# Kernel tuning notes

Hardware: AMD Instinct MI355X
Metric: run time of the kernel (lower is better)

## Reference

```python
import jax, jax.numpy as jnp
import numpy as np

B, S, D, H = 2, 2048, 1024, 16
DH = D // H
CBS, STRIDE = 32, 16      # compress block size / sliding stride
NSEL = 16                 # num_selected_blocks
WIN = 16                  # sliding_window_size (half-width)
SCALE = DH ** -0.5


def setup_inputs() -> dict:
    key = jax.random.key(0)
    ks = jax.random.split(key, 12)
    s = 0.02
    return {
        "x": jax.random.normal(ks[0], (B, S, D), jnp.float32),
        "qkv_w": jax.random.normal(ks[1], (D, 3 * D), jnp.float32) * s,
        "qkv_b": jnp.zeros((3 * D,), jnp.float32),
        "c1_w": jax.random.normal(ks[2], (CBS * D, D), jnp.float32) * s,
        "c1_b": jnp.zeros((D,), jnp.float32),
        "c2_w": jax.random.normal(ks[3], (D, D), jnp.float32) * s,
        "c2_b": jnp.zeros((D,), jnp.float32),
        "score_w": jax.random.normal(ks[4], (D, 1), jnp.float32) * s,
        "score_b": jnp.zeros((1,), jnp.float32),
        "out_w": jax.random.normal(ks[5], (D, D), jnp.float32) * s,
        "out_b": jnp.zeros((D,), jnp.float32),
    }


def reference(x, qkv_w, qkv_b, c1_w, c1_b, c2_w, c2_b, score_w, score_b, out_w, out_b):
    # q, k, v: [B, H, S, DH]
    qkv = (x @ qkv_w + qkv_b).reshape(B, S, 3, H, DH).transpose(2, 0, 3, 1, 4)
    q, k, v = qkv[0], qkv[1], qkv[2]

    # --- token compression: overlapping blocks -> MLP ---
    starts = jnp.arange(0, S - CBS + 1, STRIDE)                 # [nb]
    blk_idx = starts[:, None] + jnp.arange(CBS)[None, :]        # [nb, CBS]
    blocks = x[:, blk_idx, :].reshape(B, starts.shape[0], CBS * D)
    hidden = jax.nn.relu(blocks @ c1_w + c1_b)
    compressed = hidden @ c2_w + c2_b                           # [B, nb, D]

    # --- block selection via learned scores + top-k ---
    scores = (compressed @ score_w + score_b)[..., 0]           # [B, nb]
    _, top_idx = jax.lax.top_k(scores, NSEL)                    # [B, NSEL]
    selected = jnp.take_along_axis(compressed, top_idx[:, :, None], axis=1)  # [B, NSEL, D]

    sqkv = (selected @ qkv_w + qkv_b).reshape(B, NSEL, 3, H, DH).transpose(2, 0, 3, 1, 4)
    sel_k, sel_v = sqkv[1], sqkv[2]                             # [B, H, NSEL, DH]

    # --- sliding-window local attention (vectorized gather of banded K/V) ---
    offs = jnp.arange(-WIN, WIN + 1)                            # [2W+1]
    pos = jnp.arange(S)[:, None] + offs[None, :]                # [S, 2W+1]
    valid = (pos >= 0) & (pos < S)
    pos_c = jnp.clip(pos, 0, S - 1)
    kw = k[:, :, pos_c, :]                                      # [B, H, S, 2W+1, DH]
    vw = v[:, :, pos_c, :]
    sc = jnp.einsum('bhsd,bhswd->bhsw', q, kw) * SCALE
    sc = jnp.where(valid[None, None], sc, -jnp.inf)
    local = jnp.einsum('bhsw,bhswd->bhsd', jax.nn.softmax(sc, axis=-1), vw)

    # --- global attention over selected compressed blocks ---
    gsc = jnp.einsum('bhsd,bhkd->bhsk', q, sel_k) * SCALE       # [B, H, S, NSEL]
    glob = jnp.einsum('bhsk,bhkd->bhsd', jax.nn.softmax(gsc, axis=-1), sel_v)

    out = (local + glob).transpose(0, 2, 1, 3).reshape(B, S, D)
    return out @ out_w + out_b
```

## Files before the change

### kernel.cpp

```cpp
#include <hip/hip_runtime.h>
#include <math.h>

#define BB   2
#define SS   2048
#define DD   1024
#define HH   16
#define DH   64
#define CBS  32
#define STRIDEC 16
#define NBLK 127
#define NSEL 16
#define WIN  16
#define NW   33
#define SCALE 0.125f
#define MC   254

typedef _Float16 f16;
typedef __attribute__((ext_vector_type(8))) _Float16 f16x8;
typedef __attribute__((ext_vector_type(4))) _Float16 f16x4;
typedef __attribute__((ext_vector_type(2))) _Float16 h2;
typedef __attribute__((ext_vector_type(4))) float f32x4;

__global__ __launch_bounds__(256) void convert_f16(
    const float* __restrict__ src, f16* __restrict__ dst, int n)
{
    const int i = (blockIdx.x * 256 + threadIdx.x) * 4;
    if (i >= n) return;
    float4 v = *(const float4*)(src + i);
    f16x4 o;
    o[0] = (f16)v.x; o[1] = (f16)v.y; o[2] = (f16)v.z; o[3] = (f16)v.w;
    *(f16x4*)(dst + i) = o;
}

__global__ __launch_bounds__(256) void transpose_conv(
    const float* __restrict__ src, f16* __restrict__ dst, int K, int N)
{
    __shared__ float t[32][33];
    const int n0 = blockIdx.x * 32, k0 = blockIdx.y * 32;
    const int tx = threadIdx.x & 31, ty = threadIdx.x >> 5;
#pragma unroll
    for (int r = 0; r < 32; r += 8)
        t[ty + r][tx] = src[(size_t)(k0 + ty + r) * N + n0 + tx];
    __syncthreads();
#pragma unroll
    for (int r = 0; r < 32; r += 8)
        dst[(size_t)(n0 + ty + r) * K + k0 + tx] = (f16)t[tx][ty + r];
}

template<int OUT16>
__global__ __launch_bounds__(256) void gemm_f16(
    const f16* __restrict__ A, const f16* __restrict__ Bt,
    const float* __restrict__ bias, float* __restrict__ C,
    int M, int N, int K)
{
    constexpr int BK = 64;
    __shared__ f16 As[128 * BK];
    __shared__ f16 Bs[128 * BK];
    const int tid  = threadIdx.x;
    const int wid  = tid >> 6, lane = tid & 63;
    const int bm = blockIdx.y * 128, bn = blockIdx.x * 128;
    const int wm = (wid >> 1) * 64, wn = (wid & 1) * 64;

    const int lrow = lane >> 3;
    const int lk8  = (lane & 7) * 8;

    f32x4 acc[4][4];
#pragma unroll
    for (int i = 0; i < 4; ++i)
#pragma unroll
        for (int j = 0; j < 4; ++j) acc[i][j] = (f32x4){0.f, 0.f, 0.f, 0.f};

    for (int kt = 0; kt < K; kt += BK) {
#pragma unroll
        for (int c = 0; c < 4; ++c) {
            const int seg = c * 4 + wid;
            const int row = seg * 8 + lrow;
            const f16* ga = A + (size_t)(bm + row) * K + kt + lk8;
            __builtin_amdgcn_global_load_lds(
                (const __attribute__((address_space(1))) void*)(const void*)ga,
                (__attribute__((address_space(3))) void*)(void*)(As + seg * 512),
                16, 0, 0);
            const f16* gb = Bt + (size_t)(bn + row) * K + kt + lk8;
            __builtin_amdgcn_global_load_lds(
                (const __attribute__((address_space(1))) void*)(const void*)gb,
                (__attribute__((address_space(3))) void*)(void*)(Bs + seg * 512),
                16, 0, 0);
        }
        __syncthreads();

#pragma unroll
        for (int kk = 0; kk < 2; ++kk) {
            const int ko = kk * 32 + (lane >> 4) * 8;
            f16x8 a[4], b[4];
#pragma unroll
            for (int i = 0; i < 4; ++i)
                a[i] = *(const f16x8*)(As + (wm + i * 16 + (lane & 15)) * BK + ko);
#pragma unroll
            for (int j = 0; j < 4; ++j)
                b[j] = *(const f16x8*)(Bs + (wn + j * 16 + (lane & 15)) * BK + ko);
#pragma unroll
            for (int i = 0; i < 4; ++i)
#pragma unroll
                for (int j = 0; j < 4; ++j)
                    acc[i][j] = __builtin_amdgcn_mfma_f32_16x16x32_f16(
                        a[i], b[j], acc[i][j], 0, 0, 0);
        }
        __syncthreads();
    }

    const int rr0 = (lane >> 4) * 4;
    const int cc  = lane & 15;
#pragma unroll
    for (int i = 0; i < 4; ++i) {
        const int r = bm + wm + i * 16 + rr0;
#pragma unroll
        for (int j = 0; j < 4; ++j) {
            const int cn = bn + wn + j * 16 + cc;
            const float bv = bias[cn];
#pragma unroll
            for (int q = 0; q < 4; ++q) {
                if constexpr (OUT16)
                    ((f16*)C)[(size_t)(r + q) * N + cn] = (f16)(acc[i][j][q] + bv);
                else
                    C[(size_t)(r + q) * N + cn] = acc[i][j][q] + bv;
            }
        }
    }
}

#define C1_NZ 32
#define C1_KCHUNK 1024

__global__ __launch_bounds__(512) void gemm_c1(
    const f16* __restrict__ xh, const float* __restrict__ c1w,
    float* __restrict__ P)
{
    constexpr int BK = 64;
    constexpr int BSTR = 72;
    __shared__ f16 As[256 * BK];
    __shared__ f16 Bs[64 * BSTR];
    const int tid  = threadIdx.x;
    const int wid  = tid >> 6, lane = tid & 63;
    const int bn = blockIdx.x * 64;
    const int z  = blockIdx.z;
    const int wm = wid * 32;

    const int lrow = lane >> 3;
    const int lk8  = (lane & 7) * 8;

    f32x4 acc[2][4];
#pragma unroll
    for (int i = 0; i < 2; ++i)
#pragma unroll
        for (int j = 0; j < 4; ++j) acc[i][j] = (f32x4){0.f, 0.f, 0.f, 0.f};

    for (int t = 0; t < C1_KCHUNK / BK; ++t) {
        const int ktg = z * C1_KCHUNK + t * BK;
        const int kc  = (ktg + lk8) >> 10;
        const int kd  = (ktg + lk8) & 1023;
#pragma unroll
        for (int c = 0; c < 4; ++c) {
            const int seg = c * 8 + wid;
            int row = seg * 8 + lrow;
            if (row > MC - 1) row = MC - 1;
            const int b   = (row >= NBLK) ? 1 : 0;
            const int blk = row - b * NBLK;
            const f16* ga = xh + ((size_t)(b * SS + blk * STRIDEC + kc) << 10) + kd;
            __builtin_amdgcn_global_load_lds(
                (const __attribute__((address_space(1))) void*)(const void*)ga,
                (__attribute__((address_space(3))) void*)(void*)(As + seg * 512),
                16, 0, 0);
        }
        {
            const int kk0 = (tid >> 4) * 2;
            const int n4  = (tid & 15) * 4;
            const float* gB = c1w + (size_t)(ktg + kk0) * DD + bn + n4;
            float4 r0 = *(const float4*)gB;
            float4 r1 = *(const float4*)(gB + DD);
            const float a0[4] = {r0.x, r0.y, r0.z, r0.w};
            const float a1[4] = {r1.x, r1.y, r1.z, r1.w};
#pragma unroll
            for (int u = 0; u < 4; ++u) {
                const int n = n4 + u;
                h2 w; w[0] = (f16)a0[u]; w[1] = (f16)a1[u];
                *(h2*)&Bs[n * BSTR + (kk0 ^ (((n >> 3) & 3) << 3))] = w;
            }
        }
        __syncthreads();

#pragma unroll
        for (int kk = 0; kk < 2; ++kk) {
            const int ko = kk * 32 + (lane >> 4) * 8;
            f16x8 a[2], b[4];
#pragma unroll
            for (int i = 0; i < 2; ++i)
                a[i] = *(const f16x8*)(As + (wm + i * 16 + (lane & 15)) * BK + ko);
#pragma unroll
            for (int j = 0; j < 4; ++j) {
                const int n = j * 16 + (lane & 15);
                b[j] = *(const f16x8*)&Bs[n * BSTR + (ko ^ (((n >> 3) & 3) << 3))];
            }
#pragma unroll
            for (int i = 0; i < 2; ++i)
#pragma unroll
                for (int j = 0; j < 4; ++j)
                    acc[i][j] = __builtin_amdgcn_mfma_f32_16x16x32_f16(
                        a[i], b[j], acc[i][j], 0, 0, 0);
        }
        __syncthreads();
    }

    const int rr0 = (lane >> 4) * 4;
    const int cc  = lane & 15;
#pragma unroll
    for (int i = 0; i < 2; ++i) {
        const int r = wm + i * 16 + rr0;
#pragma unroll
        for (int j = 0; j < 4; ++j) {
            const int cn = bn + j * 16 + cc;
#pragma unroll
            for (int q = 0; q < 4; ++q)
                if (r + q < MC)
                    P[((size_t)z * MC + r + q) * DD + cn] = acc[i][j][q];
        }
    }
}

template<int MODE>
__global__ __launch_bounds__(256) void gemm128(
    const float* __restrict__ A, const float* __restrict__ Bm,
    const float* __restrict__ bias, float* __restrict__ C,
    int M, int N, int K, const int* __restrict__ selIdx, int flags)
{
    __shared__ float As[8][132];
    __shared__ float Bs[8][132];

    const int tid = threadIdx.x;
    const int bm = blockIdx.y * 128;
    const int bn = blockIdx.x * 128;
    const int nz = gridDim.z;
    const int z  = blockIdx.z;
    const int kchunk = K / nz;
    const int k0 = z * kchunk;
    const int kend = k0 + kchunk;

    const int tx = tid & 15;
    const int ty = tid >> 4;

    const int arow = tid >> 1;
    const int akq  = (tid & 1) * 4;
    const int bkr  = tid >> 5;
    const int bcol = (tid & 31) * 4;

    float acc[2][2][4][4];
#pragma unroll
    for (int qi = 0; qi < 2; ++qi)
#pragma unroll
        for (int qj = 0; qj < 2; ++qj)
#pragma unroll
            for (int i = 0; i < 4; ++i)
#pragma unroll
                for (int j = 0; j < 4; ++j) acc[qi][qj][i][j] = 0.f;

    auto loadA = [&](int kt) -> float4 {
        float4 av = make_float4(0.f, 0.f, 0.f, 0.f);
        const int grow = bm + arow;
        if (grow < M) {
            if constexpr (MODE == 0) {
                av = *(const float4*)(A + (size_t)grow * K + kt + akq);
            } else {
                const int b = grow >> 4;
                const int j = grow & 15;
                const int idx = selIdx[b * NSEL + j];
                av = *(const float4*)(A + (size_t)(b * NBLK + idx) * K + kt + akq);
            }
        }
        return av;
    };
    auto loadB = [&](int kt) -> float4 {
        return *(const float4*)(Bm + (size_t)(kt + bkr) * N + bn + bcol);
    };

    float4 av = loadA(k0);
    float4 bv = loadB(k0);

    for (int kt = k0; kt < kend; kt += 8) {
        As[akq + 0][arow] = av.x;
        As[akq + 1][arow] = av.y;
        As[akq + 2][arow] = av.z;
        As[akq + 3][arow] = av.w;
        *(float4*)&Bs[bkr][bcol] = bv;
        __syncthreads();
        if (kt + 8 < kend) {
            av = loadA(kt + 8);
            bv = loadB(kt + 8);
        }
#pragma unroll
        for (int k = 0; k < 8; ++k) {
            const float4 a0 = *(const float4*)&As[k][ty * 4];
            const float4 a1 = *(const float4*)&As[k][64 + ty * 4];
            const float4 b0 = *(const float4*)&Bs[k][tx * 4];
            const float4 b1 = *(const float4*)&Bs[k][64 + tx * 4];
            const float ar[2][4] = {{a0.x, a0.y, a0.z, a0.w},
                                    {a1.x, a1.y, a1.z, a1.w}};
            const float br[2][4] = {{b0.x, b0.y, b0.z, b0.w},
                                    {b1.x, b1.y, b1.z, b1.w}};
#pragma unroll
            for (int qi = 0; qi < 2; ++qi)
#pragma unroll
                for (int i = 0; i < 4; ++i)
#pragma unroll
                    for (int qj = 0; qj < 2; ++qj)
#pragma unroll
                        for (int j = 0; j < 4; ++j)
                            acc[qi][qj][i][j] += ar[qi][i] * br[qj][j];
        }
        __syncthreads();
    }

    if (nz == 1) {
        const bool hasB   = (flags & 1) != 0;
        const bool doRelu = (flags & 2) != 0;
#pragma unroll
        for (int qi = 0; qi < 2; ++qi)
#pragma unroll
            for (int i = 0; i < 4; ++i) {
                const int r = bm + qi * 64 + ty * 4 + i;
                if (r >= M) continue;
#pragma unroll
                for (int qj = 0; qj < 2; ++qj)
#pragma unroll
                    for (int j = 0; j < 4; ++j) {
                        const int cn = bn + qj * 64 + tx * 4 + j;
                        float v = acc[qi][qj][i][j];
                        if (hasB) v += bias[cn];
                        if (doRelu) v = fmaxf(v, 0.f);
                        C[(size_t)r * N + cn] = v;
                    }
            }
    } else {
        float* P = C + (size_t)z * M * N;
#pragma unroll
        for (int qi = 0; qi < 2; ++qi)
#pragma unroll
            for (int i = 0; i < 4; ++i) {
                const int r = bm + qi * 64 + ty * 4 + i;
                if (r >= M) continue;
#pragma unroll
                for (int qj = 0; qj < 2; ++qj)
#pragma unroll
                    for (int j = 0; j < 4; ++j) {
                        const int cn = bn + qj * 64 + tx * 4 + j;
                        P[(size_t)r * N + cn] = acc[qi][qj][i][j];
                    }
            }
    }
}

__global__ __launch_bounds__(256) void reduce_partials(
    const float* __restrict__ P, const float* __restrict__ bias,
    float* __restrict__ outp, int MN, int N, int nz, int doRelu, int halfOut)
{
    const int i = blockIdx.x * 256 + threadIdx.x;
    if (i >= MN) return;
    float s = 0.f;
    for (int z = 0; z < nz; ++z) s += P[(size_t)z * MN + i];
    s += bias[i % N];
    if (doRelu) s = fmaxf(s, 0.f);
    if (halfOut) ((f16*)outp)[i] = (f16)s;
    else         outp[i] = s;
}

__global__ __launch_bounds__(256) void w2s_kernel(
    const float* __restrict__ c2w, const float* __restrict__ sw,
    float* __restrict__ w2s)
{
    const int k = blockIdx.x;
    const float* rp = c2w + (size_t)k * DD;
    float s = 0.f;
    for (int n = threadIdx.x; n < DD; n += 256) s += rp[n] * sw[n];
#pragma unroll
    for (int off = 32; off >= 1; off >>= 1) s += __shfl_xor(s, off);
    __shared__ float red[4];
    if ((threadIdx.x & 63) == 0) red[threadIdx.x >> 6] = s;
    __syncthreads();
    if (threadIdx.x == 0) w2s[k] = red[0] + red[1] + red[2] + red[3];
}

__global__ __launch_bounds__(256) void score2_kernel(
    const float* __restrict__ hidden, const float* __restrict__ w2s,
    float* __restrict__ scores)
{
    const int row = blockIdx.x;
    const float* hp = hidden + (size_t)row * DD;
    float s = 0.f;
    for (int k = threadIdx.x; k < DD; k += 256) s += hp[k] * w2s[k];
#pragma unroll
    for (int off = 32; off >= 1; off >>= 1) s += __shfl_xor(s, off);
    __shared__ float red[4];
    if ((threadIdx.x & 63) == 0) red[threadIdx.x >> 6] = s;
    __syncthreads();
    if (threadIdx.x == 0) scores[row] = red[0] + red[1] + red[2] + red[3];
}

__global__ __launch_bounds__(128) void topk_kernel(
    const float* __restrict__ scores, int* __restrict__ top)
{
    const int b = blockIdx.x;
    const int t = threadIdx.x;
    __shared__ float sval[128];
    __shared__ float sv2[128];
    __shared__ int   si2[128];
    __shared__ unsigned char used[128];
    sval[t] = (t < NBLK) ? scores[b * NBLK + t] : -INFINITY;
    used[t] = 0;
    __syncthreads();
    for (int j = 0; j < NSEL; ++j) {
        sv2[t] = used[t] ? -INFINITY : sval[t];
        si2[t] = t;
        __syncthreads();
        for (int stp = 64; stp >= 1; stp >>= 1) {
            if (t < stp) {
                if (sv2[t + stp] > sv2[t] ||
                    (sv2[t + stp] == sv2[t] && si2[t + stp] < si2[t])) {
                    sv2[t] = sv2[t + stp];
                    si2[t] = si2[t + stp];
                }
            }
            __syncthreads();
        }
        if (t == 0) { top[b * NSEL + j] = si2[0]; used[si2[0]] = 1; }
        __syncthreads();
    }
}

#define QT 64
#define KROWS 96
#define KST2 72
#define VST 136
#define PST 136

__global__ __launch_bounds__(256) void attn_mfma(
    const f16* __restrict__ qkv, const f16* __restrict__ sqkv,
    f16* __restrict__ attn)
{
    __shared__ f16 Kl[KROWS][KST2];
    __shared__ f16 sKl[NSEL][KST2];
    __shared__ f16 Vt[DH][VST];
    __shared__ f16 Pl[4][16][PST];

    int bid = blockIdx.x;
    bid = (bid & 7) * (gridDim.x >> 3) + (bid >> 3);
    const int t = bid & 31;
    const int h = (bid >> 5) & (HH - 1);
    const int b = bid >> 9;
    const int s0 = t * QT;

    const int tid = threadIdx.x;
    const int wid = tid >> 6, lane = tid & 63;
    const int l15 = lane & 15, lg = lane >> 4;

    for (int i = tid; i < KROWS * 8; i += 256) {
        const int row = i >> 3, c8 = (i & 7) * 8;
        const int pos = s0 - WIN + row;
        f16x8 kv, vv;
#pragma unroll
        for (int u = 0; u < 8; ++u) { kv[u] = (f16)0.f; vv[u] = (f16)0.f; }
        if (pos >= 0 && pos < SS) {
            const f16* base = qkv + (size_t)(b * SS + pos) * (3 * DD) + h * DH + c8;
            kv = *(const f16x8*)(base + DD);
            vv = *(const f16x8*)(base + 2 * DD);
        }
        *(f16x8*)&Kl[row][c8] = kv;
#pragma unroll
        for (int u = 0; u < 8; ++u) Vt[c8 + u][row] = vv[u];
    }
    if (tid < NSEL * 8) {
        const int si = tid >> 3, c8 = (tid & 7) * 8;
        const f16* base = sqkv + (size_t)(b * NSEL + si) * (3 * DD) + h * DH + c8;
        f16x8 kv = *(const f16x8*)(base + DD);
        f16x8 vv = *(const f16x8*)(base + 2 * DD);
        *(f16x8*)&sKl[si][c8] = kv;
#pragma unroll
        for (int u = 0; u < 8; ++u) Vt[c8 + u][96 + si] = vv[u];
    }
    for (int i = tid; i < DH * 16; i += 256)
        Vt[i >> 4][112 + (i & 15)] = (f16)0.f;

    f16x8 qf[2];
    {
        const f16* qp = qkv + (size_t)(b * SS + s0 + wid * 16 + l15) * (3 * DD)
                      + h * DH + lg * 8;
        qf[0] = *(const f16x8*)(qp);
        qf[1] = *(const f16x8*)(qp + 32);
    }
    __syncthreads();

    f32x4 aqk[6], asel;
#pragma unroll
    for (int i = 0; i < 6; ++i) aqk[i] = (f32x4){0.f, 0.f, 0.f, 0.f};
    asel = (f32x4){0.f, 0.f, 0.f, 0.f};
#pragma unroll
    for (int kc = 0; kc < 2; ++kc) {
        const int ko = kc * 32 + lg * 8;
#pragma unroll
        for (int kvb = 0; kvb < 6; ++kvb) {
            f16x8 ka = *(const f16x8*)&Kl[kvb * 16 + l15][ko];
            aqk[kvb] = __builtin_amdgcn_mfma_f32_16x16x32_f16(ka, qf[kc], aqk[kvb], 0, 0, 0);
        }
        f16x8 ks = *(const f16x8*)&sKl[l15][ko];
        asel = __builtin_amdgcn_mfma_f32_16x16x32_f16(ks, qf[kc], asel, 0, 0, 0);
    }

    const int qt_ = wid * 16 + l15;
    float sc[6][4];
    float m = -INFINITY;
#pragma unroll
    for (int kvb = 0; kvb < 6; ++kvb)
#pragma unroll
        for (int r = 0; r < 4; ++r) {
            const int kv  = kvb * 16 + lg * 4 + r;
            const int pos = s0 - WIN + kv;
            const int dlt = kv - qt_;
            const bool ok = (dlt >= 0) & (dlt <= 32) & (pos >= 0) & (pos < SS);
            sc[kvb][r] = ok ? aqk[kvb][r] * SCALE : -INFINITY;
            m = fmaxf(m, sc[kvb][r]);
        }
    m = fmaxf(m, __shfl_xor(m, 16));
    m = fmaxf(m, __shfl_xor(m, 32));
    float sum = 0.f;
#pragma unroll
    for (int kvb = 0; kvb < 6; ++kvb)
#pragma unroll
        for (int r = 0; r < 4; ++r) {
            sc[kvb][r] = __expf(sc[kvb][r] - m);
            sum += sc[kvb][r];
        }
    sum += __shfl_xor(sum, 16);
    sum += __shfl_xor(sum, 32);
    const float inv1 = 1.f / sum;

    float s2[4];
    float m2 = -INFINITY;
#pragma unroll
    for (int r = 0; r < 4; ++r) { s2[r] = asel[r] * SCALE; m2 = fmaxf(m2, s2[r]); }
    m2 = fmaxf(m2, __shfl_xor(m2, 16));
    m2 = fmaxf(m2, __shfl_xor(m2, 32));
    float sum2 = 0.f;
#pragma unroll
    for (int r = 0; r < 4; ++r) { s2[r] = __expf(s2[r] - m2); sum2 += s2[r]; }
    sum2 += __shfl_xor(sum2, 16);
    sum2 += __shfl_xor(sum2, 32);
    const float inv2 = 1.f / sum2;

#pragma unroll
    for (int kvb = 0; kvb < 6; ++kvb) {
        h2 p01, p23;
        p01[0] = (f16)(sc[kvb][0] * inv1); p01[1] = (f16)(sc[kvb][1] * inv1);
        p23[0] = (f16)(sc[kvb][2] * inv1); p23[1] = (f16)(sc[kvb][3] * inv1);
        *(h2*)&Pl[wid][l15][kvb * 16 + lg * 4]     = p01;
        *(h2*)&Pl[wid][l15][kvb * 16 + lg * 4 + 2] = p23;
    }
    {
        h2 g01, g23, z0;
        g01[0] = (f16)(s2[0] * inv2); g01[1] = (f16)(s2[1] * inv2);
        g23[0] = (f16)(s2[2] * inv2); g23[1] = (f16)(s2[3] * inv2);
        z0[0] = (f16)0.f; z0[1] = (f16)0.f;
        *(h2*)&Pl[wid][l15][96 + lg * 4]      = g01;
        *(h2*)&Pl[wid][l15][96 + lg * 4 + 2]  = g23;
        *(h2*)&Pl[wid][l15][112 + lg * 4]     = z0;
        *(h2*)&Pl[wid][l15][112 + lg * 4 + 2] = z0;
    }

    f32x4 ov[4];
#pragma unroll
    for (int i = 0; i < 4; ++i) ov[i] = (f32x4){0.f, 0.f, 0.f, 0.f};
#pragma unroll
    for (int kc = 0; kc < 4; ++kc) {
        const int ko = kc * 32 + lg * 8;
        f16x8 pa = *(const f16x8*)&Pl[wid][l15][ko];
#pragma unroll
        for (int db = 0; db < 4; ++db) {
            f16x8 vb = *(const f16x8*)&Vt[db * 16 + l15][ko];
            ov[db] = __builtin_amdgcn_mfma_f32_16x16x32_f16(pa, vb, ov[db], 0, 0, 0);
        }
    }

    const size_t rbase = (size_t)(b * SS + s0 + wid * 16 + lg * 4);
#pragma unroll
    for (int r = 0; r < 4; ++r) {
        f16* op = attn + (rbase + r) * DD + h * DH + l15;
#pragma unroll
        for (int db = 0; db < 4; ++db)
            op[db * 16] = (f16)ov[db][r];
    }
}

extern "C" void kernel_launch(void* const* d_in, const int* in_sizes, int n_in,
                              void* d_out, int out_size, void* d_ws, size_t ws_size,
                              hipStream_t stream)
{
    const float* x       = (const float*)d_in[0];
    const float* qkv_w   = (const float*)d_in[1];
    const float* qkv_b   = (const float*)d_in[2];
    const float* c1_w    = (const float*)d_in[3];
    const float* c1_b    = (const float*)d_in[4];
    const float* c2_w    = (const float*)d_in[5];
    const float* c2_b    = (const float*)d_in[6];
    const float* score_w = (const float*)d_in[7];
    const float* score_b = (const float*)d_in[8];
    const float* out_w   = (const float*)d_in[9];
    const float* out_b   = (const float*)d_in[10];
    float* out = (float*)d_out;
    float* ws  = (float*)d_ws;
    (void)score_b;

    f16*   xh      = (f16*)ws;
    float* A1      = ws + 2097152;
    f16*   qkvb    = (f16*)A1;
    f16*   attnf   = (f16*)(A1 + 12582912);
    float* A2      = ws + 18874368;
    float* part    = A2;
    f16*   qkv_wT  = (f16*)A2;
    f16*   out_wT  = (f16*)(A2 + 1572864);
    float* hidden  = ws + 23035904;
    float* scores  = hidden + 260096;
    int*   topIdx  = (int*)(scores + 256);
    float* sqkvb   = scores + 256 + 64;
    float* w2s     = sqkvb + 49152;
    float* compSel = w2s + 1024;
    float* partC1  = ws + 24000000;

    const int MROWS = BB * SS;
    const int MSEL  = BB * NSEL;

    convert_f16<<<(MROWS * DD) / (256 * 4), 256, 0, stream>>>(x, xh, MROWS * DD);

    gemm_c1<<<dim3(DD / 64, 1, C1_NZ), 512, 0, stream>>>(xh, c1_w, partC1);

    reduce_partials<<<(MC * DD) / 256, 256, 0, stream>>>(
        partC1, c1_b, hidden, MC * DD, DD, C1_NZ, 1, 0);

    w2s_kernel<<<DD, 256, 0, stream>>>(c2_w, score_w, w2s);

    score2_kernel<<<MC, 256, 0, stream>>>(hidden, w2s, scores);

    topk_kernel<<<BB, 128, 0, stream>>>(scores, topIdx);

    gemm128<2><<<dim3(DD / 128, 1, 16), 256, 0, stream>>>(
        hidden, c2_w, nullptr, part, MSEL, DD, DD, topIdx, 0);

    reduce_partials<<<(MSEL * DD) / 256, 256, 0, stream>>>(
        part, c2_b, compSel, MSEL * DD, DD, 16, 0, 0);

    gemm128<0><<<dim3(3 * DD / 128, 1, 16), 256, 0, stream>>>(
        compSel, qkv_w, nullptr, part, MSEL, 3 * DD, DD, nullptr, 0);

    reduce_partials<<<(MSEL * 3 * DD + 255) / 256, 256, 0, stream>>>(
        part, qkv_b, sqkvb, MSEL * 3 * DD, 3 * DD, 16, 0, 1);

    transpose_conv<<<dim3(3 * DD / 32, DD / 32), 256, 0, stream>>>(
        qkv_w, qkv_wT, DD, 3 * DD);
    transpose_conv<<<dim3(DD / 32, DD / 32), 256, 0, stream>>>(
        out_w, out_wT, DD, DD);

    gemm_f16<1><<<dim3(3 * DD / 128, MROWS / 128), 256, 0, stream>>>(
        xh, qkv_wT, qkv_b, (float*)qkvb, MROWS, 3 * DD, DD);

    attn_mfma<<<BB * HH * (SS / QT), 256, 0, stream>>>(
        qkvb, (const f16*)sqkvb, attnf);

    gemm_f16<0><<<dim3(DD / 128, MROWS / 128), 256, 0, stream>>>(
        attnf, out_wT, out_b, out, MROWS, DD, DD);
}
```

Before: 220.4 us.

## Double-buffer the c1 compression GEMM with a smaller K tile and an XOR swizzle

Reworks the gemm_c1 main loop so shared-memory tiles are double-buffered. The next K tile's A loads (global_load_lds) and B loads are issued before the MFMA compute on the current buffer, which overlaps memory latency with math and removes one barrier per iteration. BK drops from 64 to 32, source row addresses are precomputed once, and the A and B shared-memory layouts use a new XOR swizzle to avoid bank conflicts. The cost is twice as many loop iterations with less work each and extra register pressure from the prefetched B values.

```diff
diff --git a/kernel.cpp b/kernel.cpp
--- a/kernel.cpp
+++ b/kernel.cpp
@@ -135,18 +135,31 @@
     const f16* __restrict__ xh, const float* __restrict__ c1w,
     float* __restrict__ P)
 {
-    constexpr int BK = 64;
-    constexpr int BSTR = 72;
-    __shared__ f16 As[256 * BK];
-    __shared__ f16 Bs[64 * BSTR];
+    constexpr int BK   = 32;
+    constexpr int BSTR = 40;
+    __shared__ f16 As[2][256 * BK];
+    __shared__ f16 Bs[2][64 * BSTR];
     const int tid  = threadIdx.x;
     const int wid  = tid >> 6, lane = tid & 63;
     const int bn = blockIdx.x * 64;
     const int z  = blockIdx.z;
     const int wm = wid * 32;
-
-    const int lrow = lane >> 3;
-    const int lk8  = (lane & 7) * 8;
+    const int l15 = lane & 15, lg = lane >> 4;
+
+    const int koff_log = ((lane & 3) ^ ((lane >> 2) & 3)) * 8;
+    int asrc_row[2];
+#pragma unroll
+    for (int c = 0; c < 2; ++c) {
+        const int seg = c * 8 + wid;
+        int row = seg * 16 + (lane >> 2);
+        if (row > MC - 1) row = MC - 1;
+        const int b   = (row >= NBLK) ? 1 : 0;
+        const int blk = row - b * NBLK;
+        asrc_row[c] = b * SS + blk * STRIDEC + z;
+    }
+
+    const int bkk = tid >> 4;
+    const int bn4 = (tid & 15) * 4;
 
     f32x4 acc[2][4];
 #pragma unroll
@@ -154,64 +167,71 @@
 #pragma unroll
         for (int j = 0; j < 4; ++j) acc[i][j] = (f32x4){0.f, 0.f, 0.f, 0.f};
 
-    for (int t = 0; t < C1_KCHUNK / BK; ++t) {
-        const int ktg = z * C1_KCHUNK + t * BK;
-        const int kc  = (ktg + lk8) >> 10;
-        const int kd  = (ktg + lk8) & 1023;
-#pragma unroll
-        for (int c = 0; c < 4; ++c) {
+    auto stageA = [&](int t, int buf) {
+#pragma unroll
+        for (int c = 0; c < 2; ++c) {
             const int seg = c * 8 + wid;
-            int row = seg * 8 + lrow;
-            if (row > MC - 1) row = MC - 1;
-            const int b   = (row >= NBLK) ? 1 : 0;
-            const int blk = row - b * NBLK;
-            const f16* ga = xh + ((size_t)(b * SS + blk * STRIDEC + kc) << 10) + kd;
+            const f16* ga = xh + ((size_t)asrc_row[c] << 10) + t * BK + koff_log;
             __builtin_amdgcn_global_load_lds(
                 (const __attribute__((address_space(1))) void*)(const void*)ga,
-                (__attribute__((address_space(3))) void*)(void*)(As + seg * 512),
+                (__attribute__((address_space(3))) void*)(void*)(&As[buf][seg * 512]),
                 16, 0, 0);
         }
-        {
-            const int kk0 = (tid >> 4) * 2;
-            const int n4  = (tid & 15) * 4;
-            const float* gB = c1w + (size_t)(ktg + kk0) * DD + bn + n4;
-            float4 r0 = *(const float4*)gB;
-            float4 r1 = *(const float4*)(gB + DD);
-            const float a0[4] = {r0.x, r0.y, r0.z, r0.w};
-            const float a1[4] = {r1.x, r1.y, r1.z, r1.w};
-#pragma unroll
-            for (int u = 0; u < 4; ++u) {
-                const int n = n4 + u;
-                h2 w; w[0] = (f16)a0[u]; w[1] = (f16)a1[u];
-                *(h2*)&Bs[n * BSTR + (kk0 ^ (((n >> 3) & 3) << 3))] = w;
-            }
-        }
+    };
+    auto loadB = [&](int t) -> float4 {
+        return *(const float4*)(c1w +
+            (size_t)(z * C1_KCHUNK + t * BK + bkk) * DD + bn + bn4);
+    };
+    auto writeB = [&](float4 v, int buf) {
+        const float a[4] = {v.x, v.y, v.z, v.w};
+#pragma unroll
+        for (int u = 0; u < 4; ++u) {
+            const int n = bn4 + u;
+            Bs[buf][n * BSTR + (bkk ^ (((n >> 2) & 3) << 3))] = (f16)a[u];
+        }
+    };
+    auto compute = [&](int buf) {
+        f16x8 a[2], b[4];
+#pragma unroll
+        for (int i = 0; i < 2; ++i) {
+            const int row = wm + i * 16 + l15;
+            a[i] = *(const f16x8*)&As[buf][row * BK + ((lg * 8) ^ ((l15 & 3) << 3))];
+        }
+#pragma unroll
+        for (int j = 0; j < 4; ++j) {
+            const int n = j * 16 + l15;
+            b[j] = *(const f16x8*)&Bs[buf][n * BSTR +
+                                           ((lg * 8) ^ (((l15 >> 2) & 3) << 3))];
+        }
+#pragma unroll
+        for (int i = 0; i < 2; ++i)
+#pragma unroll
+            for (int j = 0; j < 4; ++j)
+                acc[i][j] = __builtin_amdgcn_mfma_f32_16x16x32_f16(
+                    a[i], b[j], acc[i][j], 0, 0, 0);
+    };
+
+    stageA(0, 0);
+    writeB(loadB(0), 0);
+    __syncthreads();
+
+    int cb = 0;
+    for (int t = 0; t < C1_KCHUNK / BK; ++t) {
+        const int nb = cb ^ 1;
+        const bool pre = (t + 1 < C1_KCHUNK / BK);
+        float4 bv;
+        if (pre) {
+            stageA(t + 1, nb);
+            bv = loadB(t + 1);
+        }
+        compute(cb);
+        if (pre) writeB(bv, nb);
         __syncthreads();
-
-#pragma unroll
-        for (int kk = 0; kk < 2; ++kk) {
-            const int ko = kk * 32 + (lane >> 4) * 8;
-            f16x8 a[2], b[4];
-#pragma unroll
-            for (int i = 0; i < 2; ++i)
-                a[i] = *(const f16x8*)(As + (wm + i * 16 + (lane & 15)) * BK + ko);
-#pragma unroll
-            for (int j = 0; j < 4; ++j) {
-                const int n = j * 16 + (lane & 15);
-                b[j] = *(const f16x8*)&Bs[n * BSTR + (ko ^ (((n >> 3) & 3) << 3))];
-            }
-#pragma unroll
-            for (int i = 0; i < 2; ++i)
-#pragma unroll
-                for (int j = 0; j < 4; ++j)
-                    acc[i][j] = __builtin_amdgcn_mfma_f32_16x16x32_f16(
-                        a[i], b[j], acc[i][j], 0, 0, 0);
-        }
-        __syncthreads();
-    }
-
-    const int rr0 = (lane >> 4) * 4;
-    const int cc  = lane & 15;
+        cb = nb;
+    }
+
+    const int rr0 = lg * 4;
+    const int cc  = l15;
 #pragma unroll
     for (int i = 0; i < 2; ++i) {
         const int r = wm + i * 16 + rr0;
```

Measured after the change: 235.3 us. +6.8%, slower.

## Merge c1 compression GEMM and QKV projection GEMM into one launch

Applied to the files above, without the earlier changes.

Fuses the split-K c1 compression GEMM and the main QKV projection GEMM into a single kernel. The block index selects which GEMM a block runs, so the two independent GEMMs share one grid and can occupy the GPU together instead of running back to back. The QKV branch uses 512 threads with a 128x256 tile. To make the fusion possible, the weight transposes are moved earlier and qkv_wT/out_wT are relocated in the workspace so they do not alias the partial buffers. The cost is a larger shared-memory footprint and register pressure set by the heavier branch, which may lower occupancy for the c1 blocks.

```diff
diff --git a/kernel.cpp b/kernel.cpp
--- a/kernel.cpp
+++ b/kernel.cpp
@@ -131,97 +131,174 @@
 #define C1_NZ 32
 #define C1_KCHUNK 1024
 
-__global__ __launch_bounds__(512) void gemm_c1(
+__global__ __launch_bounds__(512) void fat_c1_qkv(
     const f16* __restrict__ xh, const float* __restrict__ c1w,
-    float* __restrict__ P)
-{
-    constexpr int BK = 64;
-    constexpr int BSTR = 72;
-    __shared__ f16 As[256 * BK];
-    __shared__ f16 Bs[64 * BSTR];
+    float* __restrict__ P,
+    const f16* __restrict__ Btq, const float* __restrict__ biasq,
+    f16* __restrict__ Cq)
+{
+    __shared__ __align__(16) f16 sh[24576];
     const int tid  = threadIdx.x;
     const int wid  = tid >> 6, lane = tid & 63;
-    const int bn = blockIdx.x * 64;
-    const int z  = blockIdx.z;
-    const int wm = wid * 32;
-
+    const int l15  = lane & 15, lg = lane >> 4;
     const int lrow = lane >> 3;
     const int lk8  = (lane & 7) * 8;
 
-    f32x4 acc[2][4];
-#pragma unroll
-    for (int i = 0; i < 2; ++i)
-#pragma unroll
-        for (int j = 0; j < 4; ++j) acc[i][j] = (f32x4){0.f, 0.f, 0.f, 0.f};
-
-    for (int t = 0; t < C1_KCHUNK / BK; ++t) {
-        const int ktg = z * C1_KCHUNK + t * BK;
-        const int kc  = (ktg + lk8) >> 10;
-        const int kd  = (ktg + lk8) & 1023;
-#pragma unroll
-        for (int c = 0; c < 4; ++c) {
-            const int seg = c * 8 + wid;
-            int row = seg * 8 + lrow;
-            if (row > MC - 1) row = MC - 1;
-            const int b   = (row >= NBLK) ? 1 : 0;
-            const int blk = row - b * NBLK;
-            const f16* ga = xh + ((size_t)(b * SS + blk * STRIDEC + kc) << 10) + kd;
-            __builtin_amdgcn_global_load_lds(
-                (const __attribute__((address_space(1))) void*)(const void*)ga,
-                (__attribute__((address_space(3))) void*)(void*)(As + seg * 512),
-                16, 0, 0);
-        }
-        {
-            const int kk0 = (tid >> 4) * 2;
-            const int n4  = (tid & 15) * 4;
-            const float* gB = c1w + (size_t)(ktg + kk0) * DD + bn + n4;
-            float4 r0 = *(const float4*)gB;
-            float4 r1 = *(const float4*)(gB + DD);
-            const float a0[4] = {r0.x, r0.y, r0.z, r0.w};
-            const float a1[4] = {r1.x, r1.y, r1.z, r1.w};
-#pragma unroll
-            for (int u = 0; u < 4; ++u) {
-                const int n = n4 + u;
-                h2 w; w[0] = (f16)a0[u]; w[1] = (f16)a1[u];
-                *(h2*)&Bs[n * BSTR + (kk0 ^ (((n >> 3) & 3) << 3))] = w;
-            }
-        }
-        __syncthreads();
-
-#pragma unroll
-        for (int kk = 0; kk < 2; ++kk) {
-            const int ko = kk * 32 + (lane >> 4) * 8;
-            f16x8 a[2], b[4];
-#pragma unroll
-            for (int i = 0; i < 2; ++i)
-                a[i] = *(const f16x8*)(As + (wm + i * 16 + (lane & 15)) * BK + ko);
+    if (blockIdx.x < 512) {
+        constexpr int BK = 64, BSTR = 72;
+        f16* As = sh;
+        f16* Bs = sh + 16384;
+        const int bn = (blockIdx.x & 15) * 64;
+        const int z  = blockIdx.x >> 4;
+        const int wm = wid * 32;
+
+        f32x4 acc[2][4];
+#pragma unroll
+        for (int i = 0; i < 2; ++i)
+#pragma unroll
+            for (int j = 0; j < 4; ++j) acc[i][j] = (f32x4){0.f, 0.f, 0.f, 0.f};
+
+        for (int t = 0; t < C1_KCHUNK / BK; ++t) {
+            const int ktg = z * C1_KCHUNK + t * BK;
+            const int kc  = (ktg + lk8) >> 10;
+            const int kd  = (ktg + lk8) & 1023;
+#pragma unroll
+            for (int c = 0; c < 4; ++c) {
+                const int seg = c * 8 + wid;
+                int row = seg * 8 + lrow;
+                if (row > MC - 1) row = MC - 1;
+                const int b   = (row >= NBLK) ? 1 : 0;
+                const int blk = row - b * NBLK;
+                const f16* ga = xh + ((size_t)(b * SS + blk * STRIDEC + kc) << 10) + kd;
+                __builtin_amdgcn_global_load_lds(
+                    (const __attribute__((address_space(1))) void*)(const void*)ga,
+                    (__attribute__((address_space(3))) void*)(void*)(As + seg * 512),
+                    16, 0, 0);
+            }
+            {
+                const int kk0 = (tid >> 4) * 2;
+                const int n4  = (tid & 15) * 4;
+                const float* gB = c1w + (size_t)(ktg + kk0) * DD + bn + n4;
+                float4 r0 = *(const float4*)gB;
+                float4 r1 = *(const float4*)(gB + DD);
+                const float a0[4] = {r0.x, r0.y, r0.z, r0.w};
+                const float a1[4] = {r1.x, r1.y, r1.z, r1.w};
+#pragma unroll
+                for (int u = 0; u < 4; ++u) {
+                    const int n = n4 + u;
+                    h2 w; w[0] = (f16)a0[u]; w[1] = (f16)a1[u];
+                    *(h2*)&Bs[n * BSTR + (kk0 ^ (((n >> 3) & 3) << 3))] = w;
+                }
+            }
+            __syncthreads();
+
+#pragma unroll
+            for (int kk = 0; kk < 2; ++kk) {
+                const int ko = kk * 32 + lg * 8;
+                f16x8 a[2], b[4];
+#pragma unroll
+                for (int i = 0; i < 2; ++i)
+                    a[i] = *(const f16x8*)(As + (wm + i * 16 + l15) * BK + ko);
+#pragma unroll
+                for (int j = 0; j < 4; ++j) {
+                    const int n = j * 16 + l15;
+                    b[j] = *(const f16x8*)&Bs[n * BSTR + (ko ^ (((n >> 3) & 3) << 3))];
+                }
+#pragma unroll
+                for (int i = 0; i < 2; ++i)
+#pragma unroll
+                    for (int j = 0; j < 4; ++j)
+                        acc[i][j] = __builtin_amdgcn_mfma_f32_16x16x32_f16(
+                            a[i], b[j], acc[i][j], 0, 0, 0);
+            }
+            __syncthreads();
+        }
+
+        const int rr0 = lg * 4;
+#pragma unroll
+        for (int i = 0; i < 2; ++i) {
+            const int r = wm + i * 16 + rr0;
 #pragma unroll
             for (int j = 0; j < 4; ++j) {
-                const int n = j * 16 + (lane & 15);
-                b[j] = *(const f16x8*)&Bs[n * BSTR + (ko ^ (((n >> 3) & 3) << 3))];
-            }
-#pragma unroll
-            for (int i = 0; i < 2; ++i)
+                const int cn = bn + j * 16 + l15;
+#pragma unroll
+                for (int q = 0; q < 4; ++q)
+                    if (r + q < MC)
+                        P[((size_t)z * MC + r + q) * DD + cn] = acc[i][j][q];
+            }
+        }
+    } else {
+        constexpr int BK = 64;
+        const int qid  = blockIdx.x - 512;
+        const int qbm  = qid / 12, qbn = qid % 12;
+        const int half = wid >> 2, w4 = wid & 3;
+        f16* As = sh;
+        f16* Bs = sh + 8192 + half * 8192;
+        const int bm = qbm * 128;
+        const int bn = qbn * 256 + half * 128;
+        const int wm = (w4 >> 1) * 64, wn = (w4 & 1) * 64;
+
+        f32x4 acc[4][4];
+#pragma unroll
+        for (int i = 0; i < 4; ++i)
+#pragma unroll
+            for (int j = 0; j < 4; ++j) acc[i][j] = (f32x4){0.f, 0.f, 0.f, 0.f};
+
+        for (int kt = 0; kt < DD; kt += BK) {
+#pragma unroll
+            for (int c = 0; c < 2; ++c) {
+                const int seg = c * 8 + wid;
+                const int row = seg * 8 + lrow;
+                const f16* ga = xh + (size_t)(bm + row) * DD + kt + lk8;
+                __builtin_amdgcn_global_load_lds(
+                    (const __attribute__((address_space(1))) void*)(const void*)ga,
+                    (__attribute__((address_space(3))) void*)(void*)(As + seg * 512),
+                    16, 0, 0);
+            }
+#pragma unroll
+            for (int c = 0; c < 4; ++c) {
+                const int seg = c * 4 + w4;
+                const int row = seg * 8 + lrow;
+                const f16* gb = Btq + (size_t)(bn + row) * DD + kt + lk8;
+                __builtin_amdgcn_global_load_lds(
+                    (const __attribute__((address_space(1))) void*)(const void*)gb,
+                    (__attribute__((address_space(3))) void*)(void*)(Bs + seg * 512),
+                    16, 0, 0);
+            }
+            __syncthreads();
+
+#pragma unroll
+            for (int kk = 0; kk < 2; ++kk) {
+                const int ko = kk * 32 + lg * 8;
+                f16x8 a[4], b[4];
+#pragma unroll
+                for (int i = 0; i < 4; ++i)
+                    a[i] = *(const f16x8*)(As + (wm + i * 16 + l15) * BK + ko);
 #pragma unroll
                 for (int j = 0; j < 4; ++j)
-                    acc[i][j] = __builtin_amdgcn_mfma_f32_16x16x32_f16(
-                        a[i], b[j], acc[i][j], 0, 0, 0);
-        }
-        __syncthreads();
-    }
-
-    const int rr0 = (lane >> 4) * 4;
-    const int cc  = lane & 15;
-#pragma unroll
-    for (int i = 0; i < 2; ++i) {
-        const int r = wm + i * 16 + rr0;
-#pragma unroll
-        for (int j = 0; j < 4; ++j) {
-            const int cn = bn + j * 16 + cc;
-#pragma unroll
-            for (int q = 0; q < 4; ++q)
-                if (r + q < MC)
-                    P[((size_t)z * MC + r + q) * DD + cn] = acc[i][j][q];
+                    b[j] = *(const f16x8*)(Bs + (wn + j * 16 + l15) * BK + ko);
+#pragma unroll
+                for (int i = 0; i < 4; ++i)
+#pragma unroll
+                    for (int j = 0; j < 4; ++j)
+                        acc[i][j] = __builtin_amdgcn_mfma_f32_16x16x32_f16(
+                            a[i], b[j], acc[i][j], 0, 0, 0);
+            }
+            __syncthreads();
+        }
+
+        const int rr0 = lg * 4;
+#pragma unroll
+        for (int i = 0; i < 4; ++i) {
+            const int r = bm + wm + i * 16 + rr0;
+#pragma unroll
+            for (int j = 0; j < 4; ++j) {
+                const int cn = bn + wn + j * 16 + l15;
+                const float bv = biasq[cn];
+#pragma unroll
+                for (int q = 0; q < 4; ++q)
+                    Cq[(size_t)(r + q) * (3 * DD) + cn] = (f16)(acc[i][j][q] + bv);
+            }
         }
     }
 }
@@ -621,8 +698,6 @@
     f16*   attnf   = (f16*)(A1 + 12582912);
     float* A2      = ws + 18874368;
     float* part    = A2;
-    f16*   qkv_wT  = (f16*)A2;
-    f16*   out_wT  = (f16*)(A2 + 1572864);
     float* hidden  = ws + 23035904;
     float* scores  = hidden + 260096;
     int*   topIdx  = (int*)(scores + 256);
@@ -630,42 +705,42 @@
     float* w2s     = sqkvb + 49152;
     float* compSel = w2s + 1024;
     float* partC1  = ws + 24000000;
+    f16*   qkv_wT  = (f16*)(ws + 33000000);
+    f16*   out_wT  = (f16*)(ws + 34600000);
 
     const int MROWS = BB * SS;
     const int MSEL  = BB * NSEL;
 
     convert_f16<<<(MROWS * DD) / (256 * 4), 256, 0, stream>>>(x, xh, MROWS * DD);
-
-    gemm_c1<<<dim3(DD / 64, 1, C1_NZ), 512, 0, stream>>>(xh, c1_w, partC1);
-
-    reduce_partials<<<(MC * DD) / 256, 256, 0, stream>>>(
-        partC1, c1_b, hidden, MC * DD, DD, C1_NZ, 1, 0);
-
-    w2s_kernel<<<DD, 256, 0, stream>>>(c2_w, score_w, w2s);
-
-    score2_kernel<<<MC, 256, 0, stream>>>(hidden, w2s, scores);
-
-    topk_kernel<<<BB, 128, 0, stream>>>(scores, topIdx);
-
-    gemm128<2><<<dim3(DD / 128, 1, 16), 256, 0, stream>>>(
-        hidden, c2_w, nullptr, part, MSEL, DD, DD, topIdx, 0);
-
-    reduce_partials<<<(MSEL * DD) / 256, 256, 0, stream>>>(
-        part, c2_b, compSel, MSEL * DD, DD, 16, 0, 0);
-
-    gemm128<0><<<dim3(3 * DD / 128, 1, 16), 256, 0, stream>>>(
-        compSel, qkv_w, nullptr, part, MSEL, 3 * DD, DD, nullptr, 0);
-
-    reduce_partials<<<(MSEL * 3 * DD + 255) / 256, 256, 0, stream>>>(
-        part, qkv_b, sqkvb, MSEL * 3 * DD, 3 * DD, 16, 0, 1);
 
     transpose_conv<<<dim3(3 * DD / 32, DD / 32), 256, 0, stream>>>(
         qkv_w, qkv_wT, DD, 3 * DD);
     transpose_conv<<<dim3(DD / 32, DD / 32), 256, 0, stream>>>(
         out_w, out_wT, DD, DD);
 
-    gemm_f16<1><<<dim3(3 * DD / 128, MROWS / 128), 256, 0, stream>>>(
-        xh, qkv_wT, qkv_b, (float*)qkvb, MROWS, 3 * DD, DD);
+    fat_c1_qkv<<<512 + 384, 512, 0, stream>>>(
+        xh, c1_w, partC1, qkv_wT, qkv_b, qkvb);
+
+    reduce_partials<<<(MC * DD) / 256, 256, 0, stream>>>(
+        partC1, c1_b, hidden, MC * DD, DD, C1_NZ, 1, 0);
+
+    w2s_kernel<<<DD, 256, 0, stream>>>(c2_w, score_w, w2s);
+
+    score2_kernel<<<MC, 256, 0, stream>>>(hidden, w2s, scores);
+
+    topk_kernel<<<BB, 128, 0, stream>>>(scores, topIdx);
+
+    gemm128<2><<<dim3(DD / 128, 1, 16), 256, 0, stream>>>(
+        hidden, c2_w, nullptr, part, MSEL, DD, DD, topIdx, 0);
+
+    reduce_partials<<<(MSEL * DD) / 256, 256, 0, stream>>>(
+        part, c2_b, compSel, MSEL * DD, DD, 16, 0, 0);
+
+    gemm128<0><<<dim3(3 * DD / 128, 1, 16), 256, 0, stream>>>(
+        compSel, qkv_w, nullptr, part, MSEL, 3 * DD, DD, nullptr, 0);
+
+    reduce_partials<<<(MSEL * 3 * DD + 255) / 256, 256, 0, stream>>>(
+        part, qkv_b, sqkvb, MSEL * 3 * DD, 3 * DD, 16, 0, 1);
 
     attn_mfma<<<BB * HH * (SS / QT), 256, 0, stream>>>(
         qkvb, (const f16*)sqkvb, attnf);
```

Measured after the change: 242.9 us. +10.2%, slower.
